# Kernel tuning notes

Measured on AMD Instinct MI355X. Metric: run time of the kernel, lower is better.

The kernel has to match this reference:

```python
import jax, jax.numpy as jnp
import numpy as np

D = 768      # embedding_dim
H = 12       # num_heads
HS = D // H  # head_size = 64
B, T, TC = 8, 1024, 256
FF = 4 * D
EPS = 1e-5


def _layernorm(x, w, b):
    mu = jnp.mean(x, axis=-1, keepdims=True)
    var = jnp.mean((x - mu) ** 2, axis=-1, keepdims=True)
    return (x - mu) / jnp.sqrt(var + EPS) * w + b


def _mha(x_q, x_kv, Wq, bq, Wk, bk, Wv, bv):
    # Batched equivalent of the per-head Python loop: weights stacked as [H, D, HS].
    q = jnp.einsum('btd,hde->bhte', x_q, Wq) + bq[None, :, None, :]
    k = jnp.einsum('bsd,hde->bhse', x_kv, Wk) + bk[None, :, None, :]
    v = jnp.einsum('bsd,hde->bhse', x_kv, Wv) + bv[None, :, None, :]
    scale = HS ** (-0.5)  # original scales by C**-0.5 with C = head_size
    wei = jax.nn.softmax(jnp.einsum('bhte,bhse->bhts', q, k) * scale, axis=-1)
    o = jnp.einsum('bhts,bhse->bhte', wei, v)  # [B,H,T,HS]
    # torch.cat over heads on dim=-1 == transpose then merge head dims
    return o.transpose(0, 2, 1, 3).reshape(o.shape[0], o.shape[2], H * HS)


def setup_inputs() -> dict:
    key = jax.random.key(0)
    ks = jax.random.split(key, 20)
    s = 0.02
    inp = {
        'img_embedding': jax.random.normal(ks[0], (B, T, D), jnp.float32),
        'context': jax.random.normal(ks[1], (B, TC, D), jnp.float32),
        'ln1_w': jnp.ones((D,), jnp.float32), 'ln1_b': jnp.zeros((D,), jnp.float32),
        'sWq': jax.random.normal(ks[2], (H, D, HS), jnp.float32) * s,
        'sbq': jnp.zeros((H, HS), jnp.float32),
        'sWk': jax.random.normal(ks[3], (H, D, HS), jnp.float32) * s,
        'sbk': jnp.zeros((H, HS), jnp.float32),
        'sWv': jax.random.normal(ks[4], (H, D, HS), jnp.float32) * s,
        'sbv': jnp.zeros((H, HS), jnp.float32),
        'ln2_w': jnp.ones((D,), jnp.float32), 'ln2_b': jnp.zeros((D,), jnp.float32),
        'cWq': jax.random.normal(ks[5], (H, D, HS), jnp.float32) * s,
        'cbq': jnp.zeros((H, HS), jnp.float32),
        'cWk': jax.random.normal(ks[6], (H, D, HS), jnp.float32) * s,
        'cbk': jnp.zeros((H, HS), jnp.float32),
        'cWv': jax.random.normal(ks[7], (H, D, HS), jnp.float32) * s,
        'cbv': jnp.zeros((H, HS), jnp.float32),
        'ln3_w': jnp.ones((D,), jnp.float32), 'ln3_b': jnp.zeros((D,), jnp.float32),
        'W1': jax.random.normal(ks[8], (D, FF), jnp.float32) * s,
        'b1': jnp.zeros((FF,), jnp.float32),
        'W2': jax.random.normal(ks[9], (FF, D), jnp.float32) * s,
        'b2': jnp.zeros((D,), jnp.float32),
    }
    return inp


def reference(img_embedding, context, ln1_w, ln1_b, sWq, sbq, sWk, sbk, sWv, sbv,
              ln2_w, ln2_b, cWq, cbq, cWk, cbk, cWv, cbv, ln3_w, ln3_b,
              W1, b1, W2, b2):
    x = img_embedding
    x = x + _mha(_layernorm(x, ln1_w, ln1_b), _layernorm(x, ln1_w, ln1_b),
                 sWq, sbq, sWk, sbk, sWv, sbv)
    x = x + _mha(_layernorm(x, ln2_w, ln2_b), context,
                 cWq, cbq, cWk, cbk, cWv, cbv)
    h = _layernorm(x, ln3_w, ln3_b)
    ff = jax.nn.silu(h @ W1 + b1) @ W2 + b2
    return x + ff
```

## Files before the change

kernel.cpp:

```cpp
#include <hip/hip_runtime.h>
#include <hip/hip_bf16.h>


#define D_EMB 768
#define N_HEADS 12
#define HEAD 64
#define B_SZ 8
#define T_IMG 1024
#define T_CTX 256
#define FF_DIM 3072
#define ROWS_IMG (B_SZ * T_IMG)
#define ROWS_CTX (B_SZ * T_CTX)
#define BIGCOL (1 << 28)

typedef __bf16 bf16x8 __attribute__((ext_vector_type(8)));
typedef __bf16 bf16x4 __attribute__((ext_vector_type(4)));
typedef float f32x4 __attribute__((ext_vector_type(4)));

__device__ __forceinline__ void gld16(const void* g, void* l) {
    __builtin_amdgcn_global_load_lds(
        (const __attribute__((address_space(1))) unsigned int*)g,
        (__attribute__((address_space(3))) unsigned int*)l, 16, 0, 0);
}

__global__ __launch_bounds__(256) void cvt_bf16_kernel(const float* __restrict__ src,
                                                       __bf16* __restrict__ dst, int n4) {
    int i = blockIdx.x * 256 + threadIdx.x;
    if (i >= n4) return;
    float4 v = ((const float4*)src)[i];
    __bf16* d = dst + i * 4;
    d[0] = (__bf16)v.x; d[1] = (__bf16)v.y; d[2] = (__bf16)v.z; d[3] = (__bf16)v.w;
}

__global__ __launch_bounds__(256) void transpose_cvt_kernel(
    const float* __restrict__ src, __bf16* __restrict__ dst,
    int src_rows, int src_cols) {
    __shared__ float tile[64][65];
    int tid = threadIdx.x;
    int r0 = blockIdx.y * 64, c0 = blockIdx.x * 64;
    int lr = tid >> 4, lc = (tid & 15) * 4;
#pragma unroll
    for (int i = 0; i < 4; i++) {
        float4 v = *(const float4*)&src[(size_t)(r0 + i * 16 + lr) * src_cols + c0 + lc];
        tile[i * 16 + lr][lc] = v.x; tile[i * 16 + lr][lc + 1] = v.y;
        tile[i * 16 + lr][lc + 2] = v.z; tile[i * 16 + lr][lc + 3] = v.w;
    }
    __syncthreads();
#pragma unroll
    for (int i = 0; i < 4; i++) {
        int cc = i * 16 + lr;
        int rr = (tid & 15) * 4;
        bf16x4 o;
#pragma unroll
        for (int j = 0; j < 4; j++) o[j] = (__bf16)tile[rr + j][cc];
        *(bf16x4*)&dst[(size_t)(c0 + cc) * src_rows + r0 + rr] = o;
    }
}

__global__ __launch_bounds__(256) void repack_qkv_t_kernel(
    const float* __restrict__ Wq, const float* __restrict__ Wk, const float* __restrict__ Wv,
    const float* __restrict__ bq, const float* __restrict__ bk, const float* __restrict__ bv,
    __bf16* __restrict__ Wt, float* __restrict__ bp) {
    __shared__ float tile[64][65];
    int tid = threadIdx.x;
    int which = blockIdx.y / 12, h = blockIdx.y - which * 12;
    int d0 = blockIdx.x * 64;
    const float* W = (which == 0) ? Wq : ((which == 1) ? Wk : Wv);
    const float* src = W + ((size_t)h * D_EMB + d0) * HEAD;
    int lr = tid >> 4, lc = (tid & 15) * 4;
#pragma unroll
    for (int i = 0; i < 4; i++) {
        float4 v = *(const float4*)&src[(size_t)(i * 16 + lr) * HEAD + lc];
        tile[i * 16 + lr][lc] = v.x; tile[i * 16 + lr][lc + 1] = v.y;
        tile[i * 16 + lr][lc + 2] = v.z; tile[i * 16 + lr][lc + 3] = v.w;
    }
    __syncthreads();
#pragma unroll
    for (int i = 0; i < 4; i++) {
        int e = i * 16 + lr;
        int dd = (tid & 15) * 4;
        bf16x4 o;
#pragma unroll
        for (int j = 0; j < 4; j++) o[j] = (__bf16)tile[dd + j][e];
        *(bf16x4*)&Wt[(size_t)(which * 768 + h * 64 + e) * D_EMB + d0 + dd] = o;
    }
    if (blockIdx.x == 0 && tid < 64) {
        const float* bb = (which == 0) ? bq : ((which == 1) ? bk : bv);
        bp[which * 768 + h * 64 + tid] = bb[h * 64 + tid];
    }
}

__global__ __launch_bounds__(256) void ln_kernel(const float* __restrict__ x,
                                                 const float* __restrict__ lw,
                                                 const float* __restrict__ lb,
                                                 __bf16* __restrict__ y) {
    int row = blockIdx.x;
    int tid = threadIdx.x;
    const float* xr = x + (size_t)row * D_EMB;
    float a0 = xr[tid], a1 = xr[tid + 256], a2 = xr[tid + 512];
    float s = a0 + a1 + a2;
    float ss = a0 * a0 + a1 * a1 + a2 * a2;
#pragma unroll
    for (int off = 32; off > 0; off >>= 1) {
        s += __shfl_down(s, off, 64);
        ss += __shfl_down(ss, off, 64);
    }
    __shared__ float red[8];
    __shared__ float stats[2];
    int wv = tid >> 6, lane = tid & 63;
    if (lane == 0) { red[wv] = s; red[4 + wv] = ss; }
    __syncthreads();
    if (tid == 0) {
        float S = red[0] + red[1] + red[2] + red[3];
        float SS = red[4] + red[5] + red[6] + red[7];
        float mu = S * (1.0f / D_EMB);
        float var = SS * (1.0f / D_EMB) - mu * mu;
        stats[0] = mu;
        stats[1] = rsqrtf(var + 1e-5f);
    }
    __syncthreads();
    float mu = stats[0], rs = stats[1];
    __bf16* yr = y + (size_t)row * D_EMB;
    yr[tid]       = (__bf16)((a0 - mu) * rs * lw[tid]       + lb[tid]);
    yr[tid + 256] = (__bf16)((a1 - mu) * rs * lw[tid + 256] + lb[tid + 256]);
    yr[tid + 512] = (__bf16)((a2 - mu) * rs * lw[tid + 512] + lb[tid + 512]);
}

__device__ __forceinline__ bf16x8 lds_frag(const __bf16* h, int row, int kk, int quad) {
    int off = (kk * 32 + quad * 8) ^ ((row & 7) << 3);
    return *(const bf16x8*)&h[row * 64 + off];
}

__global__ __launch_bounds__(256) void mfma_gemm_bt(
    const __bf16* __restrict__ A, int lda,
    const __bf16* __restrict__ Bt, int ldb,
    const float* __restrict__ bias,
    __bf16* __restrict__ Cb, int ldc,
    int Kc, int act, int qlimit,
    __bf16* __restrict__ VTout, int vtok, int vcol0, int kcol0, int kcol1,
    float* __restrict__ Xres) {
    __shared__ __bf16 As[128 * 64];
    __shared__ __bf16 Bs[128 * 64];
    int tid = threadIdx.x;
    int gx = gridDim.x;
    int nwg = gx * gridDim.y;
    int orig = blockIdx.y * gx + blockIdx.x;
    int swz = (orig & 7) * (nwg >> 3) + (orig >> 3);
    int bx = swz % gx, by = swz / gx;

    int w = tid >> 6, lane = tid & 63;
    int c = lane & 15, quad = lane >> 4;
    int wm = (w >> 1) * 64, wn = (w & 1) * 64;

    f32x4 acc[4][4];
#pragma unroll
    for (int i = 0; i < 4; i++)
#pragma unroll
        for (int j = 0; j < 4; j++) acc[i][j] = (f32x4){0.f, 0.f, 0.f, 0.f};

    int srow = tid >> 3;
    int scol = ((tid & 7) * 8) ^ ((srow & 7) * 8);
    const __bf16* Ag = A + (size_t)(by * 128 + srow) * lda + scol;
    const __bf16* Bg = Bt + (size_t)(bx * 128 + srow) * ldb + scol;
    char* AsB = (char*)As + w * 1024;
    char* BsB = (char*)Bs + w * 1024;

    for (int k0 = 0; k0 < Kc; k0 += 64) {
#pragma unroll
        for (int j = 0; j < 4; j++) {
            gld16(Ag + (size_t)(j * 32) * lda + k0, AsB + j * 4096);
            gld16(Bg + (size_t)(j * 32) * ldb + k0, BsB + j * 4096);
        }
        __syncthreads();
#pragma unroll
        for (int kk = 0; kk < 2; kk++) {
            bf16x8 af[4], bfr[4];
#pragma unroll
            for (int mi = 0; mi < 4; mi++)
                af[mi] = lds_frag(As, wm + mi * 16 + c, kk, quad);
#pragma unroll
            for (int ni = 0; ni < 4; ni++)
                bfr[ni] = lds_frag(Bs, wn + ni * 16 + c, kk, quad);
#pragma unroll
            for (int mi = 0; mi < 4; mi++)
#pragma unroll
                for (int ni = 0; ni < 4; ni++)
                    acc[mi][ni] = __builtin_amdgcn_mfma_f32_16x16x32_bf16(
                        bfr[ni], af[mi], acc[mi][ni], 0, 0, 0);
        }
        __syncthreads();
    }

#pragma unroll
    for (int mi = 0; mi < 4; mi++) {
#pragma unroll
        for (int ni = 0; ni < 4; ni++) {
            int row = by * 128 + wm + mi * 16 + c;
            int colbase = bx * 128 + wn + ni * 16 + quad * 4;
            float bvv[4] = {0.f, 0.f, 0.f, 0.f};
            if (bias) {
                float4 b4 = *(const float4*)&bias[colbase];
                bvv[0] = b4.x; bvv[1] = b4.y; bvv[2] = b4.z; bvv[3] = b4.w;
            }
            float qs = (colbase < qlimit) ? 0.125f : 1.0f;
            float v[4];
#pragma unroll
            for (int r = 0; r < 4; r++) {
                float t = (acc[mi][ni][r] + bvv[r]) * qs;
                if (act == 1) t = t / (1.0f + __expf(-t));
                v[r] = t;
            }
            if (Xres) {
                float4 x4 = *(float4*)&Xres[(size_t)row * D_EMB + colbase];
                x4.x += v[0]; x4.y += v[1]; x4.z += v[2]; x4.w += v[3];
                *(float4*)&Xres[(size_t)row * D_EMB + colbase] = x4;
            } else if (VTout && colbase >= vcol0) {
                int hc = colbase - vcol0;
                int hh = hc >> 6, ebase = hc & 63;
                int tok = row;
#pragma unroll
                for (int r = 0; r < 4; r++) {
                    int e = ebase + r;
                    int sl = ((((tok >> 3) & 7) ^ (e & 7)) << 3) | (tok & 7);
                    VTout[(size_t)(hh * 64 + e) * vtok + (tok & ~63) + sl] = (__bf16)v[r];
                }
            } else if (colbase >= kcol0 && colbase < kcol1) {
                int hc = colbase - kcol0;
                int hh = hc >> 6, ebase = hc & 63;
                int tok = row;
                int es = (((ebase >> 3) ^ (tok & 7)) << 3) | (ebase & 7);
                bf16x4 pv;
#pragma unroll
                for (int r = 0; r < 4; r++) pv[r] = (__bf16)v[r];
                *(bf16x4*)&Cb[(size_t)tok * ldc + kcol0 + hh * 64 + es] = pv;
            } else {
                bf16x4 pv;
#pragma unroll
                for (int r = 0; r < 4; r++) pv[r] = (__bf16)v[r];
                *(bf16x4*)&Cb[(size_t)row * ldc + colbase] = pv;
            }
        }
    }
}

__global__ __launch_bounds__(128, 2) void mfma_attn(
    const __bf16* __restrict__ Q, int qld,
    const __bf16* __restrict__ Kp, int kld,
    const __bf16* __restrict__ VTg, int vtok,
    int kv_tokens, float* __restrict__ X, const float* __restrict__ Xin) {
    __shared__ __bf16 Kt[64 * 64];
    __shared__ __bf16 VT[80 * 64];
    __shared__ __bf16 Ps[128 * 76];
    int tid = threadIdx.x;
    int qt = blockIdx.x & 7;
    int bh = blockIdx.x >> 3;
    int b = bh / N_HEADS, h = bh - b * N_HEADS;
    int w = tid >> 6, lane = tid & 63, c = lane & 15, quad = lane >> 4;
    int q0 = qt * 128;

    for (int i = tid; i < 16 * 64; i += 128)
        VT[64 * 64 + i] = (i < 64) ? (__bf16)1.0f : (__bf16)0.0f;

    {
        const __bf16* Qg = Q + (size_t)(b * T_IMG + q0 + (tid >> 3)) * qld
                           + h * HEAD + (tid & 7) * 8;
        char* QsB = (char*)Ps + w * 1024;
#pragma unroll
        for (int j = 0; j < 8; j++)
            gld16(Qg + (size_t)j * 16 * qld, QsB + j * 2048);
    }
    __syncthreads();
    bf16x8 qa[4][2];
#pragma unroll
    for (int st = 0; st < 4; st++)
#pragma unroll
        for (int ch = 0; ch < 2; ch++)
            qa[st][ch] = *(const bf16x8*)&Ps[(w * 64 + st * 16 + c) * 64 + ch * 32 + quad * 8];
    __syncthreads();

    f32x4 o[4][5];
#pragma unroll
    for (int st = 0; st < 4; st++)
#pragma unroll
        for (int ut = 0; ut < 5; ut++) o[st][ut] = (f32x4){0.f, 0.f, 0.f, 0.f};

    char* KtB = (char*)Kt + w * 1024;
    char* VtB = (char*)VT + w * 1024;
    int ntiles = kv_tokens >> 6;
    for (int t = 0; t < ntiles; t++) {
        const __bf16* Kg = Kp + (size_t)(b * kv_tokens + t * 64 + (tid >> 3)) * kld
                           + h * HEAD + (tid & 7) * 8;
        const __bf16* Vg = VTg + (size_t)(h * HEAD + (tid >> 3)) * vtok
                           + b * kv_tokens + t * 64 + (tid & 7) * 8;
#pragma unroll
        for (int j = 0; j < 4; j++) {
            gld16(Kg + (size_t)j * 16 * kld, KtB + j * 2048);
            gld16(Vg + (size_t)j * 16 * vtok, VtB + j * 2048);
        }
        __syncthreads();

        bf16x8 kb[4][2];
#pragma unroll
        for (int nt = 0; nt < 4; nt++)
#pragma unroll
            for (int ch = 0; ch < 2; ch++)
                kb[nt][ch] = *(const bf16x8*)&Kt[(nt * 16 + c) * 64
                                + (((ch * 4 + quad) ^ (c & 7)) << 3)];
#pragma unroll
        for (int st = 0; st < 4; st++) {
            f32x4 s[4];
#pragma unroll
            for (int nt = 0; nt < 4; nt++) {
                s[nt] = (f32x4){0.f, 0.f, 0.f, 0.f};
                s[nt] = __builtin_amdgcn_mfma_f32_16x16x32_bf16(kb[nt][0], qa[st][0], s[nt], 0, 0, 0);
                s[nt] = __builtin_amdgcn_mfma_f32_16x16x32_bf16(kb[nt][1], qa[st][1], s[nt], 0, 0, 0);
            }
#pragma unroll
            for (int nt = 0; nt < 4; nt++) {
                bf16x4 pk;
#pragma unroll
                for (int r = 0; r < 4; r++) pk[r] = (__bf16)__expf(s[nt][r]);
                *(bf16x4*)&Ps[(size_t)(w * 64 + st * 16 + c) * 76 + nt * 16 + quad * 4] = pk;
            }
        }
        __syncthreads();

        bf16x8 vb[5][2];
#pragma unroll
        for (int ut = 0; ut < 5; ut++)
#pragma unroll
            for (int ch = 0; ch < 2; ch++)
                vb[ut][ch] = *(const bf16x8*)&VT[(ut * 16 + c) * 64
                                + (((ch * 4 + quad) ^ (c & 7)) << 3)];
#pragma unroll
        for (int st = 0; st < 4; st++) {
            bf16x8 pa0 = *(const bf16x8*)&Ps[(w * 64 + st * 16 + c) * 76 + quad * 8];
            bf16x8 pa1 = *(const bf16x8*)&Ps[(w * 64 + st * 16 + c) * 76 + 32 + quad * 8];
#pragma unroll
            for (int ut = 0; ut < 5; ut++) {
                o[st][ut] = __builtin_amdgcn_mfma_f32_16x16x32_bf16(pa0, vb[ut][0], o[st][ut], 0, 0, 0);
                o[st][ut] = __builtin_amdgcn_mfma_f32_16x16x32_bf16(pa1, vb[ut][1], o[st][ut], 0, 0, 0);
            }
        }
        __syncthreads();
    }

#pragma unroll
    for (int st = 0; st < 4; st++) {
        float lr[4];
#pragma unroll
        for (int r = 0; r < 4; r++) lr[r] = __shfl(o[st][4][r], lane & 48, 64);
#pragma unroll
        for (int ut = 0; ut < 4; ut++) {
#pragma unroll
            for (int r = 0; r < 4; r++) {
                int row = b * T_IMG + q0 + w * 64 + st * 16 + quad * 4 + r;
                int col = h * HEAD + ut * 16 + c;
                size_t idx = (size_t)row * D_EMB + col;
                float base = Xin ? Xin[idx] : X[idx];
                X[idx] = base + o[st][ut][r] / lr[r];
            }
        }
    }
}

extern "C" void kernel_launch(void* const* d_in, const int* in_sizes, int n_in,
                              void* d_out, int out_size, void* d_ws, size_t ws_size,
                              hipStream_t stream) {
    const float* img  = (const float*)d_in[0];
    const float* ctx  = (const float*)d_in[1];
    const float* ln1w = (const float*)d_in[2];  const float* ln1b = (const float*)d_in[3];
    const float* sWq  = (const float*)d_in[4];  const float* sbq  = (const float*)d_in[5];
    const float* sWk  = (const float*)d_in[6];  const float* sbk  = (const float*)d_in[7];
    const float* sWv  = (const float*)d_in[8];  const float* sbv  = (const float*)d_in[9];
    const float* ln2w = (const float*)d_in[10]; const float* ln2b = (const float*)d_in[11];
    const float* cWq  = (const float*)d_in[12]; const float* cbq  = (const float*)d_in[13];
    const float* cWk  = (const float*)d_in[14]; const float* cbk  = (const float*)d_in[15];
    const float* cWv  = (const float*)d_in[16]; const float* cbv  = (const float*)d_in[17];
    const float* ln3w = (const float*)d_in[18]; const float* ln3b = (const float*)d_in[19];
    const float* W1   = (const float*)d_in[20]; const float* b1   = (const float*)d_in[21];
    const float* W2   = (const float*)d_in[22]; const float* b2   = (const float*)d_in[23];

    float* X = (float*)d_out;

    char* p = (char*)d_ws;
    __bf16* LNb  = (__bf16*)p; p += (size_t)ROWS_IMG * D_EMB * 2;
    __bf16* VTg  = (__bf16*)p; p += (size_t)12 * 64 * ROWS_IMG * 2;
    __bf16* BIG  = (__bf16*)p; p += (size_t)ROWS_IMG * FF_DIM * 2;
    __bf16* ctxb = (__bf16*)p; p += (size_t)ROWS_CTX * D_EMB * 2;
    __bf16* Wt   = (__bf16*)p; p += (size_t)2304 * 768 * 2;
    __bf16* cWt  = (__bf16*)p; p += (size_t)2304 * 768 * 2;
    __bf16* W1t  = (__bf16*)p; p += (size_t)FF_DIM * 768 * 2;
    __bf16* W2t  = (__bf16*)p; p += (size_t)768 * FF_DIM * 2;
    __bf16* VTc  = (__bf16*)p; p += (size_t)12 * 64 * ROWS_CTX * 2;
    float*  bp   = (float*)p;  p += 2304 * 4;
    float*  cbp  = (float*)p;  p += 2304 * 4;
    __bf16* QKVb = BIG;
    __bf16* Qc   = BIG;
    __bf16* KVc  = BIG + (size_t)ROWS_IMG * 768;
    __bf16* FFh  = BIG;

    cvt_bf16_kernel<<<(ROWS_CTX * D_EMB / 4 + 255) / 256, 256, 0, stream>>>(
        ctx, ctxb, ROWS_CTX * D_EMB / 4);
    repack_qkv_t_kernel<<<dim3(12, 36), 256, 0, stream>>>(
        sWq, sWk, sWv, sbq, sbk, sbv, Wt, bp);
    repack_qkv_t_kernel<<<dim3(12, 36), 256, 0, stream>>>(
        cWq, cWk, cWv, cbq, cbk, cbv, cWt, cbp);
    transpose_cvt_kernel<<<dim3(FF_DIM / 64, 768 / 64), 256, 0, stream>>>(
        W1, W1t, 768, FF_DIM);
    transpose_cvt_kernel<<<dim3(768 / 64, FF_DIM / 64), 256, 0, stream>>>(
        W2, W2t, FF_DIM, 768);

    ln_kernel<<<ROWS_IMG, 256, 0, stream>>>(img, ln1w, ln1b, LNb);
    mfma_gemm_bt<<<dim3(2304 / 128, ROWS_IMG / 128), 256, 0, stream>>>(
        LNb, D_EMB, Wt, D_EMB, bp, QKVb, 2304, D_EMB, 0, 768,
        VTg, ROWS_IMG, 1536, 768, 1536, nullptr);
    mfma_attn<<<96 * 8, 128, 0, stream>>>(
        QKVb, 2304, QKVb + 768, 2304, VTg, ROWS_IMG, T_IMG, X, img);

    ln_kernel<<<ROWS_IMG, 256, 0, stream>>>(X, ln2w, ln2b, LNb);
    mfma_gemm_bt<<<dim3(768 / 128, ROWS_IMG / 128), 256, 0, stream>>>(
        LNb, D_EMB, cWt, D_EMB, cbp, Qc, 768, D_EMB, 0, 768,
        nullptr, 0, BIGCOL, BIGCOL, BIGCOL, nullptr);
    mfma_gemm_bt<<<dim3(1536 / 128, ROWS_CTX / 128), 256, 0, stream>>>(
        ctxb, D_EMB, cWt + (size_t)768 * 768, D_EMB, cbp + 768,
        KVc, 1536, D_EMB, 0, 0,
        VTc, ROWS_CTX, 768, 0, 768, nullptr);
    mfma_attn<<<96 * 8, 128, 0, stream>>>(
        Qc, 768, KVc, 1536, VTc, ROWS_CTX, T_CTX, X, nullptr);

    ln_kernel<<<ROWS_IMG, 256, 0, stream>>>(X, ln3w, ln3b, LNb);
    mfma_gemm_bt<<<dim3(FF_DIM / 128, ROWS_IMG / 128), 256, 0, stream>>>(
        LNb, D_EMB, W1t, D_EMB, b1, FFh, FF_DIM, D_EMB, 1, 0,
        nullptr, 0, BIGCOL, BIGCOL, BIGCOL, nullptr);
    mfma_gemm_bt<<<dim3(768 / 128, ROWS_IMG / 128), 256, 0, stream>>>(
        FFh, FF_DIM, W2t, FF_DIM, b2, nullptr, D_EMB, FF_DIM, 0, 0,
        nullptr, 0, BIGCOL, BIGCOL, BIGCOL, X);
}
```

Before: 476.8 us.

## Split-K the W2 GEMM into two bf16 partials plus reduce kernel; reorder attention grid

The final FF down-projection GEMM had only 6x64=384 workgroups with K=3072. It now runs as a two-way split-K over blockIdx.z, writing bf16 partials into the reused LN buffer. A new reduce kernel sums the partials with the bias and adds them into the fp32 residual. This adds partial-sum traffic, one extra launch and bf16 rounding of each partial. The attention grid mapping also now puts query tiles in the outer index, which changes scheduling locality across heads.

```diff
diff --git a/kernel.cpp b/kernel.cpp
--- a/kernel.cpp
+++ b/kernel.cpp
@@ -12,6 +12,7 @@
 #define ROWS_IMG (B_SZ * T_IMG)
 #define ROWS_CTX (B_SZ * T_CTX)
 #define BIGCOL (1 << 28)
+#define PART_STRIDE (ROWS_IMG * D_EMB)
 
 typedef __bf16 bf16x8 __attribute__((ext_vector_type(8)));
 typedef __bf16 bf16x4 __attribute__((ext_vector_type(4)));
@@ -30,6 +31,23 @@
     float4 v = ((const float4*)src)[i];
     __bf16* d = dst + i * 4;
     d[0] = (__bf16)v.x; d[1] = (__bf16)v.y; d[2] = (__bf16)v.z; d[3] = (__bf16)v.w;
+}
+
+__global__ __launch_bounds__(256) void reduce_w2_kernel(
+    const __bf16* __restrict__ P, const float* __restrict__ b2,
+    float* __restrict__ X) {
+    int i = blockIdx.x * 256 + threadIdx.x;
+    int base = i * 4;
+    int col = base % D_EMB;
+    bf16x4 p0 = *(const bf16x4*)&P[base];
+    bf16x4 p1 = *(const bf16x4*)&P[PART_STRIDE + base];
+    float4 x = *(float4*)&X[base];
+    float4 bb = *(const float4*)&b2[col];
+    x.x += (float)p0[0] + (float)p1[0] + bb.x;
+    x.y += (float)p0[1] + (float)p1[1] + bb.y;
+    x.z += (float)p0[2] + (float)p1[2] + bb.z;
+    x.w += (float)p0[3] + (float)p1[3] + bb.w;
+    *(float4*)&X[base] = x;
 }
 
 __global__ __launch_bounds__(256) void transpose_cvt_kernel(
@@ -142,6 +160,7 @@
     __shared__ __bf16 As[128 * 64];
     __shared__ __bf16 Bs[128 * 64];
     int tid = threadIdx.x;
+    int kz = blockIdx.z;
     int gx = gridDim.x;
     int nwg = gx * gridDim.y;
     int orig = blockIdx.y * gx + blockIdx.x;
@@ -160,8 +179,8 @@
 
     int srow = tid >> 3;
     int scol = ((tid & 7) * 8) ^ ((srow & 7) * 8);
-    const __bf16* Ag = A + (size_t)(by * 128 + srow) * lda + scol;
-    const __bf16* Bg = Bt + (size_t)(bx * 128 + srow) * ldb + scol;
+    const __bf16* Ag = A + (size_t)(by * 128 + srow) * lda + (size_t)kz * Kc + scol;
+    const __bf16* Bg = Bt + (size_t)(bx * 128 + srow) * ldb + (size_t)kz * Kc + scol;
     char* AsB = (char*)As + w * 1024;
     char* BsB = (char*)Bs + w * 1024;
 
@@ -198,7 +217,7 @@
             int row = by * 128 + wm + mi * 16 + c;
             int colbase = bx * 128 + wn + ni * 16 + quad * 4;
             float bvv[4] = {0.f, 0.f, 0.f, 0.f};
-            if (bias) {
+            if (bias && kz == 0) {
                 float4 b4 = *(const float4*)&bias[colbase];
                 bvv[0] = b4.x; bvv[1] = b4.y; bvv[2] = b4.z; bvv[3] = b4.w;
             }
@@ -234,10 +253,11 @@
                 for (int r = 0; r < 4; r++) pv[r] = (__bf16)v[r];
                 *(bf16x4*)&Cb[(size_t)tok * ldc + kcol0 + hh * 64 + es] = pv;
             } else {
+                __bf16* dst = Cb + (size_t)kz * PART_STRIDE;
                 bf16x4 pv;
 #pragma unroll
                 for (int r = 0; r < 4; r++) pv[r] = (__bf16)v[r];
-                *(bf16x4*)&Cb[(size_t)row * ldc + colbase] = pv;
+                *(bf16x4*)&dst[(size_t)row * ldc + colbase] = pv;
             }
         }
     }
@@ -252,8 +272,8 @@
     __shared__ __bf16 VT[80 * 64];
     __shared__ __bf16 Ps[128 * 76];
     int tid = threadIdx.x;
-    int qt = blockIdx.x & 7;
-    int bh = blockIdx.x >> 3;
+    int bh = blockIdx.x % 96;
+    int qt = blockIdx.x / 96;
     int b = bh / N_HEADS, h = bh - b * N_HEADS;
     int w = tid >> 6, lane = tid & 63, c = lane & 15, quad = lane >> 4;
     int q0 = qt * 128;
@@ -395,6 +415,7 @@
     __bf16* VTc  = (__bf16*)p; p += (size_t)12 * 64 * ROWS_CTX * 2;
     float*  bp   = (float*)p;  p += 2304 * 4;
     float*  cbp  = (float*)p;  p += 2304 * 4;
+    __bf16* Pk   = LNb;
     __bf16* QKVb = BIG;
     __bf16* Qc   = BIG;
     __bf16* KVc  = BIG + (size_t)ROWS_IMG * 768;
@@ -433,7 +454,8 @@
     mfma_gemm_bt<<<dim3(FF_DIM / 128, ROWS_IMG / 128), 256, 0, stream>>>(
         LNb, D_EMB, W1t, D_EMB, b1, FFh, FF_DIM, D_EMB, 1, 0,
         nullptr, 0, BIGCOL, BIGCOL, BIGCOL, nullptr);
-    mfma_gemm_bt<<<dim3(768 / 128, ROWS_IMG / 128), 256, 0, stream>>>(
-        FFh, FF_DIM, W2t, FF_DIM, b2, nullptr, D_EMB, FF_DIM, 0, 0,
-        nullptr, 0, BIGCOL, BIGCOL, BIGCOL, X);
-}
+    mfma_gemm_bt<<<dim3(768 / 128, ROWS_IMG / 128, 2), 256, 0, stream>>>(
+        FFh, FF_DIM, W2t, FF_DIM, nullptr, Pk, D_EMB, 1536, 0, 0,
+        nullptr, 0, BIGCOL, BIGCOL, BIGCOL, nullptr);
+    reduce_w2_kernel<<<ROWS_IMG * D_EMB / 4 / 256, 256, 0, stream>>>(Pk, b2, X);
+}
```

Result: faster. 463.7 us (-2.7%).
